# Kernel optimization log

Measured on AMD Instinct MI355X. Metric: run time of the kernel, lower is better.

The kernel has to match this reference:

```python
import jax, jax.numpy as jnp
import numpy as np

R = 50000          # residues
P = 24             # residue_pad_length
APR = 15           # atoms per residue (<= P)
N = R * APR        # total atoms
ACD = ATD = RCD = RID = 32
N_ATOM_CODES, N_ATOM_TYPES, N_RES_CODES, MAX_SEQ = 38, 6, 21, 1024
VEC_OUT, SC_OUT = 64, 256          # irreps_out = 64x1e + 256x0e
SC_IN = P * ACD + P * ATD + RCD + RID  # 1600 scalar inputs


def setup_inputs() -> dict:
    key = jax.random.key(0)
    ks = jax.random.split(key, 10)
    return {
        "residue_base_coords": jax.random.normal(ks[0], (R, 3), jnp.float32),
        "residue_relative_coords": jax.random.normal(ks[1], (N, 3), jnp.float32),
        "residue_code_index": jax.random.randint(ks[2], (R,), 0, N_RES_CODES),
        "residue_sequence_index": jnp.arange(R) % MAX_SEQ,
        "atom_code_index": jax.random.randint(ks[3], (N,), 0, N_ATOM_CODES),
        "atom_type_index": jax.random.randint(ks[4], (N,), 0, N_ATOM_TYPES),
        "residue_index_atomwise": jnp.repeat(jnp.arange(R), APR),  # sorted, APR atoms each
        "W_atom_code": jax.random.normal(ks[5], (N_ATOM_CODES, ACD), jnp.float32),
        "W_atom_type": jax.random.normal(ks[6], (N_ATOM_TYPES, ATD), jnp.float32),
        "W_res_code": jax.random.normal(ks[7], (N_RES_CODES, RCD), jnp.float32),
        "W_res_idx": jax.random.normal(ks[8], (MAX_SEQ, RID), jnp.float32),
        "W_vec": jax.random.normal(jax.random.fold_in(key, 1), (P, VEC_OUT), jnp.float32),
        "W_sc": jax.random.normal(ks[9], (SC_IN, SC_OUT), jnp.float32),
    }


def reference(residue_base_coords, residue_relative_coords, residue_code_index,
              residue_sequence_index, atom_code_index, atom_type_index,
              residue_index_atomwise, W_atom_code, W_atom_type, W_res_code,
              W_res_idx, W_vec, W_sc):
    R_ = residue_base_coords.shape[0]
    P_ = W_vec.shape[0]
    N_ = residue_index_atomwise.shape[0]
    ri = residue_index_atomwise
    # vectorized replacement of the per-residue python loop:
    # position of each atom within its residue (residue_index_atomwise is sorted)
    offsets = jnp.searchsorted(ri, jnp.arange(R_))            # first atom of each residue
    pos = jnp.arange(N_) - offsets[ri]                        # [N]
    # scatter atoms into padded [R, P, ...] layout (pad slots stay 0, like F.pad)
    mask = jnp.zeros((R_, P_), bool).at[ri, pos].set(True)
    rel = jnp.zeros((R_, P_, 3), residue_relative_coords.dtype).at[ri, pos].set(residue_relative_coords)
    codes = jnp.zeros((R_, P_), atom_code_index.dtype).at[ri, pos].set(atom_code_index)
    types = jnp.zeros((R_, P_), atom_type_index.dtype).at[ri, pos].set(atom_type_index)
    maskf = mask.astype(W_atom_code.dtype)[..., None]
    # embedding lookups, masked (pad embeddings zeroed as in the torch code)
    ac = (W_atom_code[codes] * maskf).reshape(R_, -1)         # [R, P*ACD]
    at = (W_atom_type[types] * maskf).reshape(R_, -1)         # [R, P*ATD]
    rc = W_res_code[residue_code_index]                       # [R, RCD]
    rix = W_res_idx[residue_sequence_index]                   # [R, RID]
    scalars = jnp.concatenate([ac, at, rc, rix], axis=-1)     # [R, SC_IN]
    # e3nn o3.Linear: l=1 channels mix only with l=1 (Px1e -> VEC_OUTx1e),
    # l=0 channels mix only with l=0; path-normalized by sqrt(fan_in), no bias.
    out_vec = jnp.einsum('rpc,pm->rmc', rel, W_vec) / jnp.sqrt(jnp.float32(P_))
    out_sc = (scalars @ W_sc) / jnp.sqrt(jnp.float32(scalars.shape[-1]))
    features = jnp.concatenate([out_vec.reshape(R_, -1), out_sc], axis=-1)  # [R, 3*VEC_OUT+SC_OUT]
    return residue_base_coords, features  # ResidueState(coords, features)
```

## Files before the change

kernel.cpp:

```cpp
#include <hip/hip_runtime.h>
#include <stdint.h>

static constexpr int P       = 24;
static constexpr int EMB_D   = 32;
static constexpr int N_AC    = 38;
static constexpr int N_AT    = 6;
static constexpr int N_RC    = 21;
static constexpr int MAXSEQ  = 1024;
static constexpr int VEC_OUT = 64;
static constexpr int SC_OUT  = 256;
static constexpr int FEAT    = 3 * VEC_OUT + SC_OUT;
static constexpr int CT      = N_AC * N_AT;
static constexpr int NROWS   = P * CT;
static constexpr int ROWB    = SC_OUT * 2;
static constexpr uint32_t ZROWB = (uint32_t)NROWS * ROWB;

__device__ __forceinline__ unsigned short f2bf(float f) {
    uint32_t x = __float_as_uint(f);
    uint32_t r = (x + 0x7FFFu + ((x >> 16) & 1u)) >> 16;
    return (unsigned short)r;
}

__global__ __launch_bounds__(256) void k1_init_build(
        const float* __restrict__ Wac, const float* __restrict__ Wat,
        const float* __restrict__ Wrc, const float* __restrict__ Wri,
        const float* __restrict__ Wsc,
        float* __restrict__ Ec, float* __restrict__ Et,
        float* __restrict__ Erc, float* __restrict__ Erix,
        int* __restrict__ starts, int* __restrict__ ends, int R) {
    int b = blockIdx.x;
    const int initB = (R + 255) / 256;
    if (b < initB) {
        int i = b * 256 + threadIdx.x;
        if (i < R) { starts[i] = 0; ends[i] = 0; }
        return;
    }
    b -= initB;
    const float* Wemb; float* E; int n_emb, sc_base, idx;
    if (b < P * N_AC) {
        Wemb = Wac; E = Ec; n_emb = N_AC; sc_base = 0; idx = b;
    } else if (b < P * N_AC + P * N_AT) {
        Wemb = Wat; E = Et; n_emb = N_AT; sc_base = P * EMB_D; idx = b - P * N_AC;
    } else if (b < P * N_AC + P * N_AT + N_RC) {
        Wemb = Wrc; E = Erc; n_emb = N_RC; sc_base = 2 * P * EMB_D;
        idx = b - (P * N_AC + P * N_AT);
    } else {
        Wemb = Wri; E = Erix; n_emb = MAXSEQ; sc_base = 2 * P * EMB_D + EMB_D;
        idx = b - (P * N_AC + P * N_AT + N_RC);
    }
    int p = idx / n_emb, e = idx % n_emb;
    int o = threadIdx.x;
    const float* wrow = Wemb + (size_t)e * EMB_D;
    const float* scol = Wsc + (size_t)(sc_base + p * EMB_D) * SC_OUT + o;
    float s = 0.f;
#pragma unroll
    for (int d = 0; d < EMB_D; ++d) s += wrow[d] * scol[(size_t)d * SC_OUT];
    E[(size_t)idx * SC_OUT + o] = s * 0.025f;
}

__global__ void k2_find_bounds(const int* __restrict__ ri, int* __restrict__ starts,
                               int* __restrict__ ends, int N) {
    int i = blockIdx.x * blockDim.x + threadIdx.x;
    if (i >= N) return;
    int r = ri[i];
    if (i == 0 || ri[i - 1] != r) starts[r] = i;
    if (i == N - 1 || ri[i + 1] != r) ends[r] = i + 1;
}

__global__ __launch_bounds__(256) void k3_fuse_plan(
        const float* __restrict__ Ec, const float* __restrict__ Et,
        unsigned short* __restrict__ Etab,
        const int* __restrict__ ac, const int* __restrict__ at,
        const int* __restrict__ starts, const int* __restrict__ ends,
        const float* __restrict__ rel, uint4* __restrict__ plan, int R) {
    int b = blockIdx.x;
    if (b < NROWS + 1) {
        int o = threadIdx.x;
        if (b == NROWS) { Etab[(size_t)b * SC_OUT + o] = 0; return; }
        int j = b / CT, ct = b % CT, c = ct / N_AT, t = ct % N_AT;
        float s = Ec[((size_t)j * N_AC + c) * SC_OUT + o] +
                  Et[((size_t)j * N_AT + t) * SC_OUT + o];
        Etab[(size_t)b * SC_OUT + o] = f2bf(s);
        return;
    }
    int i = (b - (NROWS + 1)) * 256 + threadIdx.x;
    if (i >= R * P) return;
    int r = i / P, s = i % P;
    int st = starts[r];
    int cnt = ends[r] - st;
    if (cnt > P) cnt = P;
    uint4 q = make_uint4(ZROWB, 0u, 0u, 0u);
    if (s < cnt) {
        int ai = st + s;
        q.x = (uint32_t)((s * CT + ac[ai] * N_AT + at[ai]) * ROWB);
        q.y = __float_as_uint(rel[(size_t)3 * ai]);
        q.z = __float_as_uint(rel[(size_t)3 * ai + 1]);
        q.w = __float_as_uint(rel[(size_t)3 * ai + 2]);
    }
    plan[i] = q;
}

__global__ __launch_bounds__(256) void k4_residue(
        const float* __restrict__ base, const int* __restrict__ rcode,
        const int* __restrict__ rseq, const int* __restrict__ starts,
        const int* __restrict__ ends, const uint4* __restrict__ plan,
        const unsigned char* __restrict__ tab, const float* __restrict__ Erc,
        const float* __restrict__ Erix, const float* __restrict__ Wvec,
        float* __restrict__ out_coords, float* __restrict__ out_feat, int R) {
    __shared__ float lds_w[P * VEC_OUT];
    for (int t = threadIdx.x; t < P * VEC_OUT; t += 256) lds_w[t] = Wvec[t];
    __syncthreads();

    int wid = (blockIdx.x << 2) + (threadIdx.x >> 6);
    int lane = threadIdx.x & 63;
    int r = __builtin_amdgcn_readfirstlane(wid);
    if (r >= R) return;

    int cnt = ends[r] - starts[r];
    if (cnt > P) cnt = P;

    float4 ea = *reinterpret_cast<const float4*>(Erc + (size_t)rcode[r] * SC_OUT + lane * 4);
    float4 eb = *reinterpret_cast<const float4*>(Erix + (size_t)rseq[r] * SC_OUT + lane * 4);
    float a0 = ea.x + eb.x, a1 = ea.y + eb.y, a2 = ea.z + eb.z, a3 = ea.w + eb.w;
    float v0 = 0.f, v1 = 0.f, v2 = 0.f;
    const int lb = lane * 8;

    float w[16];
#pragma unroll
    for (int k = 0; k < 16; ++k) w[k] = lds_w[k * VEC_OUT + lane];

    const uint4* pp = plan + (size_t)r * P;
    uint4 q[16];
#pragma unroll
    for (int k = 0; k < 16; ++k) q[k] = pp[k];

    uint2 g[16];
#pragma unroll
    for (int k = 0; k < 16; ++k)
        g[k] = *reinterpret_cast<const uint2*>(tab + q[k].x + lb);

#pragma unroll
    for (int k = 0; k < 16; ++k) {
        a0 += __uint_as_float(g[k].x << 16);
        a1 += __uint_as_float(g[k].x & 0xFFFF0000u);
        a2 += __uint_as_float(g[k].y << 16);
        a3 += __uint_as_float(g[k].y & 0xFFFF0000u);
        v0 = fmaf(__uint_as_float(q[k].y), w[k], v0);
        v1 = fmaf(__uint_as_float(q[k].z), w[k], v1);
        v2 = fmaf(__uint_as_float(q[k].w), w[k], v2);
    }
    if (cnt > 16) {
#pragma unroll
        for (int k = 16; k < P; ++k) {
            uint4 qq = pp[k];
            uint2 gg = *reinterpret_cast<const uint2*>(tab + qq.x + lb);
            float ww = lds_w[k * VEC_OUT + lane];
            a0 += __uint_as_float(gg.x << 16);
            a1 += __uint_as_float(gg.x & 0xFFFF0000u);
            a2 += __uint_as_float(gg.y << 16);
            a3 += __uint_as_float(gg.y & 0xFFFF0000u);
            v0 = fmaf(__uint_as_float(qq.y), ww, v0);
            v1 = fmaf(__uint_as_float(qq.z), ww, v1);
            v2 = fmaf(__uint_as_float(qq.w), ww, v2);
        }
    }

    const float vs = 0.20412414523193150818f;
    float* frow = out_feat + (size_t)r * FEAT;
    frow[lane * 3 + 0] = v0 * vs;
    frow[lane * 3 + 1] = v1 * vs;
    frow[lane * 3 + 2] = v2 * vs;
    *reinterpret_cast<float4*>(frow + 3 * VEC_OUT + lane * 4) =
        make_float4(a0, a1, a2, a3);
    if (lane < 3) out_coords[(size_t)r * 3 + lane] = base[(size_t)r * 3 + lane];
}

extern "C" void kernel_launch(void* const* d_in, const int* in_sizes, int n_in,
                              void* d_out, int out_size, void* d_ws, size_t ws_size,
                              hipStream_t stream) {
    const float* base  = (const float*)d_in[0];
    const float* rel   = (const float*)d_in[1];
    const int*   rcode = (const int*)d_in[2];
    const int*   rseq  = (const int*)d_in[3];
    const int*   acode = (const int*)d_in[4];
    const int*   atype = (const int*)d_in[5];
    const int*   ri    = (const int*)d_in[6];
    const float* Wac   = (const float*)d_in[7];
    const float* Wat   = (const float*)d_in[8];
    const float* Wrc   = (const float*)d_in[9];
    const float* Wri   = (const float*)d_in[10];
    const float* Wv    = (const float*)d_in[11];
    const float* Wsc   = (const float*)d_in[12];

    const int R = in_sizes[0] / 3;
    const int N = in_sizes[6];

    float* out_coords = (float*)d_out;
    float* out_feat   = out_coords + (size_t)R * 3;

    char* ws = (char*)d_ws;
    size_t ofs = 0;
    auto alloc = [&](size_t bytes) {
        void* p = ws + ofs;
        ofs = (ofs + bytes + 255) & ~255ULL;
        return p;
    };
    int*            starts = (int*)alloc((size_t)R * 4);
    int*            ends   = (int*)alloc((size_t)R * 4);
    float*          Ec_f   = (float*)alloc((size_t)P * N_AC * SC_OUT * 4);
    float*          Et_f   = (float*)alloc((size_t)P * N_AT * SC_OUT * 4);
    float*          Erc_f  = (float*)alloc((size_t)N_RC * SC_OUT * 4);
    float*          Erix_f = (float*)alloc((size_t)MAXSEQ * SC_OUT * 4);
    unsigned short* Etab   = (unsigned short*)alloc((size_t)(NROWS + 1) * SC_OUT * 2);
    uint4*          plan   = (uint4*)alloc((size_t)R * P * 16);
    (void)ws_size; (void)n_in; (void)out_size;

    const int initB  = (R + 255) / 256;
    const int k1B    = initB + P * N_AC + P * N_AT + N_RC + MAXSEQ;
    const int planB  = (R * P + 255) / 256;
    const int k3B    = (NROWS + 1) + planB;

    k1_init_build<<<k1B, 256, 0, stream>>>(Wac, Wat, Wrc, Wri, Wsc,
                                           Ec_f, Et_f, Erc_f, Erix_f, starts, ends, R);
    k2_find_bounds<<<(N + 255) / 256, 256, 0, stream>>>(ri, starts, ends, N);
    k3_fuse_plan<<<k3B, 256, 0, stream>>>(Ec_f, Et_f, Etab, acode, atype,
                                          starts, ends, rel, plan, R);
    k4_residue<<<(R + 3) / 4, 256, 0, stream>>>(
        base, rcode, rseq, starts, ends, plan, (const unsigned char*)Etab,
        Erc_f, Erix_f, Wv, out_coords, out_feat, R);
}
```

Before: 66.69 us.

## Drop per-slot plan buffer; build row offsets in-wave via readlane broadcast

Removes the intermediate R*P uint4 plan array (about 19MB written and read back) and instead has each residue wavefront load its atom codes, types and relative coords directly, one atom per lane. It broadcasts the row offsets and coords across the wave with readlane. A compact per-residue header (start, count, rcode, rseq) replaces the separate starts/ends/rcode/rseq reads. This cuts global memory traffic between the kernels, at the cost of extra scalar readlane instructions and a slightly longer dependency chain before the table gathers.

```diff
diff --git a/kernel.cpp b/kernel.cpp
--- a/kernel.cpp
+++ b/kernel.cpp
@@ -67,12 +67,12 @@
     if (i == N - 1 || ri[i + 1] != r) ends[r] = i + 1;
 }
 
-__global__ __launch_bounds__(256) void k3_fuse_plan(
+__global__ __launch_bounds__(256) void k3_fuse_hdr(
         const float* __restrict__ Ec, const float* __restrict__ Et,
         unsigned short* __restrict__ Etab,
-        const int* __restrict__ ac, const int* __restrict__ at,
         const int* __restrict__ starts, const int* __restrict__ ends,
-        const float* __restrict__ rel, uint4* __restrict__ plan, int R) {
+        const int* __restrict__ rcode, const int* __restrict__ rseq,
+        int4* __restrict__ hdr, int R) {
     int b = blockIdx.x;
     if (b < NROWS + 1) {
         int o = threadIdx.x;
@@ -84,29 +84,21 @@
         return;
     }
     int i = (b - (NROWS + 1)) * 256 + threadIdx.x;
-    if (i >= R * P) return;
-    int r = i / P, s = i % P;
-    int st = starts[r];
-    int cnt = ends[r] - st;
-    if (cnt > P) cnt = P;
-    uint4 q = make_uint4(ZROWB, 0u, 0u, 0u);
-    if (s < cnt) {
-        int ai = st + s;
-        q.x = (uint32_t)((s * CT + ac[ai] * N_AT + at[ai]) * ROWB);
-        q.y = __float_as_uint(rel[(size_t)3 * ai]);
-        q.z = __float_as_uint(rel[(size_t)3 * ai + 1]);
-        q.w = __float_as_uint(rel[(size_t)3 * ai + 2]);
-    }
-    plan[i] = q;
+    if (i >= R) return;
+    int st = starts[i];
+    int c = ends[i] - st;
+    if (c > P) c = P;
+    hdr[i] = make_int4(st, c, rcode[i], rseq[i]);
 }
 
 __global__ __launch_bounds__(256) void k4_residue(
-        const float* __restrict__ base, const int* __restrict__ rcode,
-        const int* __restrict__ rseq, const int* __restrict__ starts,
-        const int* __restrict__ ends, const uint4* __restrict__ plan,
-        const unsigned char* __restrict__ tab, const float* __restrict__ Erc,
-        const float* __restrict__ Erix, const float* __restrict__ Wvec,
-        float* __restrict__ out_coords, float* __restrict__ out_feat, int R) {
+        const float* __restrict__ base, const int4* __restrict__ hdr,
+        const int* __restrict__ acode, const int* __restrict__ atype,
+        const float* __restrict__ rel, const unsigned char* __restrict__ tab,
+        const float* __restrict__ Erc, const float* __restrict__ Erix,
+        const float* __restrict__ Wvec,
+        float* __restrict__ out_coords, float* __restrict__ out_feat,
+        int R, int N) {
     __shared__ float lds_w[P * VEC_OUT];
     for (int t = threadIdx.x; t < P * VEC_OUT; t += 256) lds_w[t] = Wvec[t];
     __syncthreads();
@@ -116,52 +108,79 @@
     int r = __builtin_amdgcn_readfirstlane(wid);
     if (r >= R) return;
 
-    int cnt = ends[r] - starts[r];
-    if (cnt > P) cnt = P;
-
-    float4 ea = *reinterpret_cast<const float4*>(Erc + (size_t)rcode[r] * SC_OUT + lane * 4);
-    float4 eb = *reinterpret_cast<const float4*>(Erix + (size_t)rseq[r] * SC_OUT + lane * 4);
+    int4 h = hdr[r];
+    const int off = h.x, cnt = h.y;
+
+    int ia = off + lane; if (ia > N - 1) ia = N - 1;
+    int code = acode[ia];
+    int type = atype[ia];
+    uint32_t rowoff = ZROWB;
+    if (lane < cnt) rowoff = (uint32_t)((lane * CT + code * N_AT + type) * ROWB);
+    int ir = 3 * off + lane; if (ir > 3 * N - 1) ir = 3 * N - 1;
+    float relv = rel[ir];
+    if (lane >= 3 * cnt) relv = 0.f;
+
+    float4 ea = *reinterpret_cast<const float4*>(Erc + (size_t)h.z * SC_OUT + lane * 4);
+    float4 eb = *reinterpret_cast<const float4*>(Erix + (size_t)h.w * SC_OUT + lane * 4);
     float a0 = ea.x + eb.x, a1 = ea.y + eb.y, a2 = ea.z + eb.z, a3 = ea.w + eb.w;
     float v0 = 0.f, v1 = 0.f, v2 = 0.f;
     const int lb = lane * 8;
 
-    float w[16];
-#pragma unroll
-    for (int k = 0; k < 16; ++k) w[k] = lds_w[k * VEC_OUT + lane];
-
-    const uint4* pp = plan + (size_t)r * P;
-    uint4 q[16];
-#pragma unroll
-    for (int k = 0; k < 16; ++k) q[k] = pp[k];
-
+    uint32_t ro[16];
+#pragma unroll
+    for (int k = 0; k < 16; ++k)
+        ro[k] = (uint32_t)__builtin_amdgcn_readlane((int)rowoff, k);
     uint2 g[16];
 #pragma unroll
     for (int k = 0; k < 16; ++k)
-        g[k] = *reinterpret_cast<const uint2*>(tab + q[k].x + lb);
-
+        g[k] = *reinterpret_cast<const uint2*>(tab + ro[k] + lb);
+
+    float rx[16], ry[16], rz[16];
 #pragma unroll
     for (int k = 0; k < 16; ++k) {
+        rx[k] = __int_as_float(__builtin_amdgcn_readlane(__float_as_int(relv), 3 * k));
+        ry[k] = __int_as_float(__builtin_amdgcn_readlane(__float_as_int(relv), 3 * k + 1));
+        rz[k] = __int_as_float(__builtin_amdgcn_readlane(__float_as_int(relv), 3 * k + 2));
+    }
+
+#pragma unroll
+    for (int k = 0; k < 16; ++k) {
+        float w = lds_w[k * VEC_OUT + lane];
         a0 += __uint_as_float(g[k].x << 16);
         a1 += __uint_as_float(g[k].x & 0xFFFF0000u);
         a2 += __uint_as_float(g[k].y << 16);
         a3 += __uint_as_float(g[k].y & 0xFFFF0000u);
-        v0 = fmaf(__uint_as_float(q[k].y), w[k], v0);
-        v1 = fmaf(__uint_as_float(q[k].z), w[k], v1);
-        v2 = fmaf(__uint_as_float(q[k].w), w[k], v2);
-    }
+        v0 = fmaf(rx[k], w, v0);
+        v1 = fmaf(ry[k], w, v1);
+        v2 = fmaf(rz[k], w, v2);
+    }
+
     if (cnt > 16) {
+        int ir2 = 3 * off + 64 + lane;
+        if (ir2 > 3 * N - 1) ir2 = 3 * N - 1;
+        float relv2 = rel[ir2];
+        if (64 + lane >= 3 * cnt) relv2 = 0.f;
 #pragma unroll
         for (int k = 16; k < P; ++k) {
-            uint4 qq = pp[k];
-            uint2 gg = *reinterpret_cast<const uint2*>(tab + qq.x + lb);
-            float ww = lds_w[k * VEC_OUT + lane];
+            uint32_t rr = (uint32_t)__builtin_amdgcn_readlane((int)rowoff, k);
+            uint2 gg = *reinterpret_cast<const uint2*>(tab + rr + lb);
+            float w = lds_w[k * VEC_OUT + lane];
+            float sx = __int_as_float(3 * k < 64
+                ? __builtin_amdgcn_readlane(__float_as_int(relv), 3 * k)
+                : __builtin_amdgcn_readlane(__float_as_int(relv2), 3 * k - 64));
+            float sy = __int_as_float(3 * k + 1 < 64
+                ? __builtin_amdgcn_readlane(__float_as_int(relv), 3 * k + 1)
+                : __builtin_amdgcn_readlane(__float_as_int(relv2), 3 * k + 1 - 64));
+            float sz = __int_as_float(3 * k + 2 < 64
+                ? __builtin_amdgcn_readlane(__float_as_int(relv), 3 * k + 2)
+                : __builtin_amdgcn_readlane(__float_as_int(relv2), 3 * k + 2 - 64));
             a0 += __uint_as_float(gg.x << 16);
             a1 += __uint_as_float(gg.x & 0xFFFF0000u);
             a2 += __uint_as_float(gg.y << 16);
             a3 += __uint_as_float(gg.y & 0xFFFF0000u);
-            v0 = fmaf(__uint_as_float(qq.y), ww, v0);
-            v1 = fmaf(__uint_as_float(qq.z), ww, v1);
-            v2 = fmaf(__uint_as_float(qq.w), ww, v2);
+            v0 = fmaf(sx, w, v0);
+            v1 = fmaf(sy, w, v1);
+            v2 = fmaf(sz, w, v2);
         }
     }
 
@@ -212,20 +231,20 @@
     float*          Erc_f  = (float*)alloc((size_t)N_RC * SC_OUT * 4);
     float*          Erix_f = (float*)alloc((size_t)MAXSEQ * SC_OUT * 4);
     unsigned short* Etab   = (unsigned short*)alloc((size_t)(NROWS + 1) * SC_OUT * 2);
-    uint4*          plan   = (uint4*)alloc((size_t)R * P * 16);
+    int4*           hdr    = (int4*)alloc((size_t)R * 16);
     (void)ws_size; (void)n_in; (void)out_size;
 
-    const int initB  = (R + 255) / 256;
-    const int k1B    = initB + P * N_AC + P * N_AT + N_RC + MAXSEQ;
-    const int planB  = (R * P + 255) / 256;
-    const int k3B    = (NROWS + 1) + planB;
+    const int initB = (R + 255) / 256;
+    const int k1B   = initB + P * N_AC + P * N_AT + N_RC + MAXSEQ;
+    const int hdrB  = (R + 255) / 256;
+    const int k3B   = (NROWS + 1) + hdrB;
 
     k1_init_build<<<k1B, 256, 0, stream>>>(Wac, Wat, Wrc, Wri, Wsc,
                                            Ec_f, Et_f, Erc_f, Erix_f, starts, ends, R);
     k2_find_bounds<<<(N + 255) / 256, 256, 0, stream>>>(ri, starts, ends, N);
-    k3_fuse_plan<<<k3B, 256, 0, stream>>>(Ec_f, Et_f, Etab, acode, atype,
-                                          starts, ends, rel, plan, R);
+    k3_fuse_hdr<<<k3B, 256, 0, stream>>>(Ec_f, Et_f, Etab, starts, ends,
+                                         rcode, rseq, hdr, R);
     k4_residue<<<(R + 3) / 4, 256, 0, stream>>>(
-        base, rcode, rseq, starts, ends, plan, (const unsigned char*)Etab,
-        Erc_f, Erix_f, Wv, out_coords, out_feat, R);
-}
+        base, hdr, acode, atype, rel, (const unsigned char*)Etab,
+        Erc_f, Erix_f, Wv, out_coords, out_feat, R, N);
+}
```

After: 63.80 us. 4.3% less time.
